# Kernel optimization log

Measured on AMD Instinct MI355X. Metric: run time of the kernel, lower is better.

The kernel has to match this reference:

```python
import jax, jax.numpy as jnp
import numpy as np

N_SRC = 50000
N_DST = 50000
E = 800000
D = 64


def setup_inputs() -> dict:
    key = jax.random.key(0)
    k1, k2, k3, k4 = jax.random.split(key, 4)
    src_emb = jax.random.normal(k1, (N_SRC, D), dtype=jnp.float32)
    e_att = jax.random.uniform(k2, (E, 1), dtype=jnp.float32)
    src_idx = jax.random.randint(k3, (E,), 0, N_SRC, dtype=jnp.int64)
    dst_idx = jax.random.randint(k4, (E,), 0, N_DST, dtype=jnp.int64)
    return {"src_emb": src_emb, "e_att": e_att, "src_idx": src_idx, "dst_idx": dst_idx}


def reference(src_emb, e_att, src_idx, dst_idx):
    # DGL: fn.src_mul_edge('emb_o','att','msg') then fn.sum('msg','emb_n')
    # msg[e] = src_emb[src_idx[e]] * e_att[e]  -> scatter-sum into dst nodes
    msg = src_emb[src_idx] * e_att                      # [E, D]
    emb_n = jax.ops.segment_sum(msg, dst_idx, num_segments=N_DST)  # [N_DST, D]
    return emb_n
```

## Files before the change

kernel.cpp:

```cpp
#include <hip/hip_runtime.h>
#include <hip/hip_fp16.h>


#define D 64
#define CAP 64
#define OVF_CAP 65536
#define NPART 8


__global__ void __launch_bounds__(256)
scatter_xcd_kernel(const int* __restrict__ dst_idx, const int* __restrict__ src_idx,
                   const float* __restrict__ e_att, int* __restrict__ cursor,
                   unsigned* __restrict__ payload,
                   int* __restrict__ ovf_count, int* __restrict__ ovf_list,
                   int E, int n_dst, int rpx, int epb) {
    int x     = blockIdx.x & (NPART - 1);
    int chunk = blockIdx.x >> 3;
    int e0 = chunk * epb;
    int e1 = min(e0 + epb, E);
    int lo = x * rpx;
    int hi = min(lo + rpx, n_dst);

    for (int e = e0 + threadIdx.x; e < e1; e += 256) {
        int d = dst_idx[e];
        if (d < lo || d >= hi) continue;
        int p = atomicAdd(&cursor[d], 1);
        if (p < CAP) {
            unsigned pl = (unsigned)src_idx[e] |
                          ((unsigned)__half_as_ushort(__float2half(e_att[e])) << 16);
            payload[(size_t)d * CAP + p] = pl;
        } else {
            int oi = atomicAdd(ovf_count, 1);
            if (oi < OVF_CAP) ovf_list[oi] = e;
        }
    }
}


__global__ void __launch_bounds__(256)
gather_xcd_kernel(const float* __restrict__ src_emb,
                  const unsigned* __restrict__ payload,
                  const int* __restrict__ cursor,
                  const int* __restrict__ dst_idx, const int* __restrict__ src_idx,
                  const float* __restrict__ e_att,
                  const int* __restrict__ ovf_count, const int* __restrict__ ovf_list,
                  float* __restrict__ out, int n_dst, int rpx) {
    int x    = blockIdx.x & (NPART - 1);
    int g    = blockIdx.x >> 3;
    int wv   = threadIdx.x >> 6;
    int lane = threadIdx.x & 63;
    int local = g * 4 + wv;
    if (local >= rpx) return;
    int w = x * rpx + local;
    if (w >= n_dst) return;

    int cn  = cursor[w];
    int cnt = min(cn, CAP);

    unsigned plv = payload[(size_t)w * CAP + lane];
    int pli = (int)plv;

    float acc = 0.f;
    int j = 0;
    for (; j + 4 <= cnt; j += 4) {
        unsigned p0 = (unsigned)__builtin_amdgcn_readlane(pli, j);
        unsigned p1 = (unsigned)__builtin_amdgcn_readlane(pli, j + 1);
        unsigned p2 = (unsigned)__builtin_amdgcn_readlane(pli, j + 2);
        unsigned p3 = (unsigned)__builtin_amdgcn_readlane(pli, j + 3);
        float a0 = __half2float(__ushort_as_half((unsigned short)(p0 >> 16)));
        float a1 = __half2float(__ushort_as_half((unsigned short)(p1 >> 16)));
        float a2 = __half2float(__ushort_as_half((unsigned short)(p2 >> 16)));
        float a3 = __half2float(__ushort_as_half((unsigned short)(p3 >> 16)));
        float v0 = src_emb[(size_t)(p0 & 0xffff) * D + lane];
        float v1 = src_emb[(size_t)(p1 & 0xffff) * D + lane];
        float v2 = src_emb[(size_t)(p2 & 0xffff) * D + lane];
        float v3 = src_emb[(size_t)(p3 & 0xffff) * D + lane];
        acc = fmaf(v0, a0, acc);
        acc = fmaf(v1, a1, acc);
        acc = fmaf(v2, a2, acc);
        acc = fmaf(v3, a3, acc);
    }
    for (; j < cnt; ++j) {
        unsigned p = (unsigned)__builtin_amdgcn_readlane(pli, j);
        float a = __half2float(__ushort_as_half((unsigned short)(p >> 16)));
        acc = fmaf(src_emb[(size_t)(p & 0xffff) * D + lane], a, acc);
    }

    if (cn > CAP) {
        int oc = *ovf_count;
        if (oc > OVF_CAP) oc = OVF_CAP;
        for (int i = 0; i < oc; ++i) {
            int e = ovf_list[i];
            if (dst_idx[e] == w) {
                float a = e_att[e];
                int   s = src_idx[e];
                acc = fmaf(src_emb[(size_t)s * D + lane], a, acc);
            }
        }
    }

    out[(size_t)w * D + lane] = acc;
}

__global__ void __launch_bounds__(256)
atomic_fallback_kernel(const float* __restrict__ src_emb, const float* __restrict__ e_att,
                       const int* __restrict__ src_idx, const int* __restrict__ dst_idx,
                       float* __restrict__ out, int E) {
    int tid  = blockIdx.x * blockDim.x + threadIdx.x;
    int e    = tid >> 4;
    int part = tid & 15;
    if (e >= E) return;
    int   s = src_idx[e];
    int   d = dst_idx[e];
    float a = e_att[e];
    float4 v = ((const float4*)src_emb)[(size_t)s * 16 + part];
    float* orow = out + (size_t)d * D + part * 4;
    atomicAdd(orow + 0, v.x * a);
    atomicAdd(orow + 1, v.y * a);
    atomicAdd(orow + 2, v.z * a);
    atomicAdd(orow + 3, v.w * a);
}

extern "C" void kernel_launch(void* const* d_in, const int* in_sizes, int n_in,
                              void* d_out, int out_size, void* d_ws, size_t ws_size,
                              hipStream_t stream) {
    const float* src_emb = (const float*)d_in[0];
    const float* e_att   = (const float*)d_in[1];
    const int*   src_idx = (const int*)d_in[2];
    const int*   dst_idx = (const int*)d_in[3];
    float*       out     = (float*)d_out;

    const int E     = in_sizes[2];
    const int n_dst = out_size / D;
    const int n_src = in_sizes[0] / D;

    size_t need_ints = (size_t)n_dst * CAP + n_dst + 1 + OVF_CAP;
    if (n_src <= 65536 && ws_size >= need_ints * sizeof(int)) {
        unsigned* payload = (unsigned*)d_ws;
        int* cursor    = (int*)d_ws + (size_t)n_dst * CAP;
        int* ovf_count = cursor + n_dst;
        int* ovf_list  = ovf_count + 1;

        hipMemsetAsync(cursor, 0, ((size_t)n_dst + 1) * sizeof(int), stream);

        const int rpx = (n_dst + NPART - 1) / NPART;
        const int chunks = 512;
        const int epb    = (E + chunks - 1) / chunks;
        scatter_xcd_kernel<<<chunks * NPART, 256, 0, stream>>>(
            dst_idx, src_idx, e_att, cursor, payload, ovf_count, ovf_list,
            E, n_dst, rpx, epb);

        const int gpb = (rpx + 3) / 4;
        gather_xcd_kernel<<<gpb * NPART, 256, 0, stream>>>(
            src_emb, payload, cursor, dst_idx, src_idx, e_att,
            ovf_count, ovf_list, out, n_dst, rpx);
        return;
    }

    hipMemsetAsync(d_out, 0, (size_t)out_size * sizeof(float), stream);
    atomic_fallback_kernel<<<(E * 16 + 255) / 256, 256, 0, stream>>>(
        src_emb, e_att, src_idx, dst_idx, out, E);
}
```

Baseline: 142.0 us.

## Pre-bin edges by destination partition and gather from half-precision embedding copy

```diff
diff --git a/kernel.cpp b/kernel.cpp
--- a/kernel.cpp
+++ b/kernel.cpp
@@ -6,52 +6,105 @@
 #define CAP 64
 #define OVF_CAP 65536
 #define NPART 8
-
-
-__global__ void __launch_bounds__(256)
-scatter_xcd_kernel(const int* __restrict__ dst_idx, const int* __restrict__ src_idx,
-                   const float* __restrict__ e_att, int* __restrict__ cursor,
-                   unsigned* __restrict__ payload,
-                   int* __restrict__ ovf_count, int* __restrict__ ovf_list,
-                   int E, int n_dst, int rpx, int epb) {
-    int x     = blockIdx.x & (NPART - 1);
+#define SCAP 512
+
+__global__ void __launch_bounds__(256)
+convert_emb_kernel(const float* __restrict__ src, __half* __restrict__ dst, int n4) {
+    int i = blockIdx.x * blockDim.x + threadIdx.x;
+    if (i >= n4) return;
+    float4 v = ((const float4*)src)[i];
+    ushort4 h;
+    h.x = __half_as_ushort(__float2half(v.x));
+    h.y = __half_as_ushort(__float2half(v.y));
+    h.z = __half_as_ushort(__float2half(v.z));
+    h.w = __half_as_ushort(__float2half(v.w));
+    ((ushort4*)dst)[i] = h;
+}
+
+__global__ void __launch_bounds__(256)
+bin8_kernel(const int* __restrict__ dst_idx, const int* __restrict__ src_idx,
+            const float* __restrict__ e_att,
+            unsigned long long* __restrict__ plist, int* __restrict__ gcur8,
+            int E, int pcap, int epb) {
+    __shared__ unsigned long long stage[NPART * SCAP];
+    __shared__ int cnt[NPART];
+    __shared__ int base_[NPART];
+    int t = threadIdx.x;
+    if (t < NPART) cnt[t] = 0;
+    __syncthreads();
+
+    int e0 = blockIdx.x * epb;
+    int e1 = min(e0 + epb, E);
+    for (int e = e0 + t; e < e1; e += 256) {
+        int d = dst_idx[e];
+        int p = d & (NPART - 1);
+        unsigned dl = (unsigned)d >> 3;
+        unsigned short a16 = __half_as_ushort(__float2half(e_att[e]));
+        unsigned long long rec = (unsigned long long)a16 << 32 |
+                                 ((unsigned)src_idx[e] | (dl << 16));
+        int slot = atomicAdd(&cnt[p], 1);
+        if (slot < SCAP) {
+            stage[p * SCAP + slot] = rec;
+        } else {
+            int g = atomicAdd(&gcur8[p], 1);
+            if (g < pcap) plist[(size_t)p * pcap + g] = rec;
+        }
+    }
+    __syncthreads();
+    if (t < NPART) base_[t] = atomicAdd(&gcur8[t], min(cnt[t], SCAP));
+    __syncthreads();
+    for (int p = 0; p < NPART; ++p) {
+        int n = min(cnt[p], SCAP);
+        unsigned long long* dstp = plist + (size_t)p * pcap + base_[p];
+        for (int i = t; i < n; i += 256)
+            __builtin_nontemporal_store(stage[p * SCAP + i], dstp + i);
+    }
+}
+
+__global__ void __launch_bounds__(256)
+scatter2_kernel(const unsigned long long* __restrict__ plist,
+                const int* __restrict__ gcur8, int* __restrict__ cursor,
+                unsigned* __restrict__ payload,
+                int* __restrict__ ovf_count, unsigned long long* __restrict__ ovf_list,
+                int pcap, int cpp) {
+    int p     = blockIdx.x & (NPART - 1);
     int chunk = blockIdx.x >> 3;
-    int e0 = chunk * epb;
-    int e1 = min(e0 + epb, E);
-    int lo = x * rpx;
-    int hi = min(lo + rpx, n_dst);
-
-    for (int e = e0 + threadIdx.x; e < e1; e += 256) {
-        int d = dst_idx[e];
-        if (d < lo || d >= hi) continue;
-        int p = atomicAdd(&cursor[d], 1);
-        if (p < CAP) {
-            unsigned pl = (unsigned)src_idx[e] |
-                          ((unsigned)__half_as_ushort(__float2half(e_att[e])) << 16);
-            payload[(size_t)d * CAP + p] = pl;
+    int len   = gcur8[p];
+    const unsigned long long* lp = plist + (size_t)p * pcap;
+    int stride = cpp * 256;
+    for (int i = chunk * 256 + threadIdx.x; i < len; i += stride) {
+        unsigned long long rec = lp[i];
+        unsigned lo  = (unsigned)rec;
+        unsigned a16 = (unsigned)(rec >> 32) & 0xffffu;
+        unsigned src = lo & 0xffffu;
+        unsigned dl  = lo >> 16;
+        int d = (int)((dl << 3) | (unsigned)p);
+        int slot = atomicAdd(&cursor[d], 1);
+        unsigned pay = (a16 << 16) | src;
+        if (slot < CAP) {
+            payload[(size_t)d * CAP + slot] = pay;
         } else {
             int oi = atomicAdd(ovf_count, 1);
-            if (oi < OVF_CAP) ovf_list[oi] = e;
+            if (oi < OVF_CAP)
+                ovf_list[oi] = ((unsigned long long)(unsigned)d << 32) | pay;
         }
     }
 }
 
-
-__global__ void __launch_bounds__(256)
-gather_xcd_kernel(const float* __restrict__ src_emb,
-                  const unsigned* __restrict__ payload,
-                  const int* __restrict__ cursor,
-                  const int* __restrict__ dst_idx, const int* __restrict__ src_idx,
-                  const float* __restrict__ e_att,
-                  const int* __restrict__ ovf_count, const int* __restrict__ ovf_list,
-                  float* __restrict__ out, int n_dst, int rpx) {
-    int x    = blockIdx.x & (NPART - 1);
+__global__ void __launch_bounds__(256)
+gather_kernel(const __half* __restrict__ emb_h,
+              const unsigned* __restrict__ payload,
+              const int* __restrict__ cursor,
+              const int* __restrict__ ovf_count,
+              const unsigned long long* __restrict__ ovf_list,
+              float* __restrict__ out, int n_dst, int rpx) {
+    int p    = blockIdx.x & (NPART - 1);
     int g    = blockIdx.x >> 3;
     int wv   = threadIdx.x >> 6;
     int lane = threadIdx.x & 63;
     int local = g * 4 + wv;
     if (local >= rpx) return;
-    int w = x * rpx + local;
+    int w = (local << 3) | p;
     if (w >= n_dst) return;
 
     int cn  = cursor[w];
@@ -71,34 +124,32 @@
         float a1 = __half2float(__ushort_as_half((unsigned short)(p1 >> 16)));
         float a2 = __half2float(__ushort_as_half((unsigned short)(p2 >> 16)));
         float a3 = __half2float(__ushort_as_half((unsigned short)(p3 >> 16)));
-        float v0 = src_emb[(size_t)(p0 & 0xffff) * D + lane];
-        float v1 = src_emb[(size_t)(p1 & 0xffff) * D + lane];
-        float v2 = src_emb[(size_t)(p2 & 0xffff) * D + lane];
-        float v3 = src_emb[(size_t)(p3 & 0xffff) * D + lane];
+        float v0 = __half2float(emb_h[(size_t)(p0 & 0xffff) * D + lane]);
+        float v1 = __half2float(emb_h[(size_t)(p1 & 0xffff) * D + lane]);
+        float v2 = __half2float(emb_h[(size_t)(p2 & 0xffff) * D + lane]);
+        float v3 = __half2float(emb_h[(size_t)(p3 & 0xffff) * D + lane]);
         acc = fmaf(v0, a0, acc);
         acc = fmaf(v1, a1, acc);
         acc = fmaf(v2, a2, acc);
         acc = fmaf(v3, a3, acc);
     }
     for (; j < cnt; ++j) {
-        unsigned p = (unsigned)__builtin_amdgcn_readlane(pli, j);
-        float a = __half2float(__ushort_as_half((unsigned short)(p >> 16)));
-        acc = fmaf(src_emb[(size_t)(p & 0xffff) * D + lane], a, acc);
+        unsigned pv = (unsigned)__builtin_amdgcn_readlane(pli, j);
+        float a = __half2float(__ushort_as_half((unsigned short)(pv >> 16)));
+        acc = fmaf(__half2float(emb_h[(size_t)(pv & 0xffff) * D + lane]), a, acc);
     }
 
     if (cn > CAP) {
-        int oc = *ovf_count;
-        if (oc > OVF_CAP) oc = OVF_CAP;
+        int oc = min(*ovf_count, OVF_CAP);
         for (int i = 0; i < oc; ++i) {
-            int e = ovf_list[i];
-            if (dst_idx[e] == w) {
-                float a = e_att[e];
-                int   s = src_idx[e];
-                acc = fmaf(src_emb[(size_t)s * D + lane], a, acc);
+            unsigned long long orec = ovf_list[i];
+            if ((int)(orec >> 32) == w) {
+                unsigned pv = (unsigned)orec;
+                float a = __half2float(__ushort_as_half((unsigned short)(pv >> 16)));
+                acc = fmaf(__half2float(emb_h[(size_t)(pv & 0xffff) * D + lane]), a, acc);
             }
         }
     }
-
     out[(size_t)w * D + lane] = acc;
 }
 
@@ -133,27 +184,45 @@
     const int E     = in_sizes[2];
     const int n_dst = out_size / D;
     const int n_src = in_sizes[0] / D;
-
-    size_t need_ints = (size_t)n_dst * CAP + n_dst + 1 + OVF_CAP;
-    if (n_src <= 65536 && ws_size >= need_ints * sizeof(int)) {
-        unsigned* payload = (unsigned*)d_ws;
-        int* cursor    = (int*)d_ws + (size_t)n_dst * CAP;
-        int* ovf_count = cursor + n_dst;
-        int* ovf_list  = ovf_count + 1;
-
-        hipMemsetAsync(cursor, 0, ((size_t)n_dst + 1) * sizeof(int), stream);
-
-        const int rpx = (n_dst + NPART - 1) / NPART;
-        const int chunks = 512;
-        const int epb    = (E + chunks - 1) / chunks;
-        scatter_xcd_kernel<<<chunks * NPART, 256, 0, stream>>>(
-            dst_idx, src_idx, e_att, cursor, payload, ovf_count, ovf_list,
-            E, n_dst, rpx, epb);
+    const int rpx   = (n_dst + NPART - 1) / NPART;
+    const int pcap  = E;
+
+    size_t off_plist = 0;
+    size_t off_ovf   = off_plist + (size_t)NPART * pcap * 8;
+    size_t off_emb   = off_ovf + (size_t)OVF_CAP * 8;
+    size_t off_pay   = off_emb + (size_t)n_src * D * 2;
+    size_t off_cur   = off_pay + (size_t)n_dst * CAP * 4;
+    size_t need      = off_cur + ((size_t)n_dst + NPART + 1) * 4;
+
+    if (n_src <= 65536 && rpx <= 8192 && ws_size >= need) {
+        char* ws = (char*)d_ws;
+        unsigned long long* plist    = (unsigned long long*)(ws + off_plist);
+        unsigned long long* ovf_list = (unsigned long long*)(ws + off_ovf);
+        __half*   emb_h   = (__half*)(ws + off_emb);
+        unsigned* payload = (unsigned*)(ws + off_pay);
+        int*      cursor  = (int*)(ws + off_cur);
+        int*      gcur8   = cursor + n_dst;
+        int*      ovf_count = gcur8 + NPART;
+
+        hipMemsetAsync(cursor, 0, ((size_t)n_dst + NPART + 1) * sizeof(int), stream);
+
+        convert_emb_kernel<<<(n_src * D / 4 + 255) / 256, 256, 0, stream>>>(
+            src_emb, emb_h, n_src * D / 4);
+
+        const int s1_blocks = 256;
+        const int epb = (E + s1_blocks - 1) / s1_blocks;
+        bin8_kernel<<<s1_blocks, 256, 0, stream>>>(dst_idx, src_idx, e_att,
+                                                   plist, gcur8, E, pcap, epb);
+
+        const int cpp = 64;
+        scatter2_kernel<<<cpp * NPART, 256, 0, stream>>>(plist, gcur8, cursor,
+                                                         payload, ovf_count,
+                                                         ovf_list, pcap, cpp);
 
         const int gpb = (rpx + 3) / 4;
-        gather_xcd_kernel<<<gpb * NPART, 256, 0, stream>>>(
-            src_emb, payload, cursor, dst_idx, src_idx, e_att,
-            ovf_count, ovf_list, out, n_dst, rpx);
+        gather_kernel<<<gpb * NPART, 256, 0, stream>>>(emb_h, payload, cursor,
+                                                       ovf_count, ovf_list,
+                                                       out, n_dst, rpx);
         return;
     }
 
```

Result: slower. 147.1 us (+3.6%).
